# Kernel optimization log

Hardware: AMD Instinct MI355X
Metric: run time of the kernel (lower is better)

The kernel has to match this reference:

```python
import jax, jax.numpy as jnp
import numpy as np

N_NODES = 50000
N_SCHEMES = 5
K = 16
HIDDEN = 128
N_CLASSES = 8


def setup_inputs() -> dict:
    key = jax.random.key(0)
    ks = jax.random.split(key, 8)
    sc_nei = jax.random.randint(ks[0], (N_SCHEMES, N_NODES, K), 0, N_NODES)
    feats = jax.random.normal(ks[1], (N_NODES, HIDDEN), dtype=jnp.float32)
    W1 = jax.random.normal(ks[2], (HIDDEN, HIDDEN), dtype=jnp.float32) * (1.0 / np.sqrt(HIDDEN))
    b1 = jnp.zeros((HIDDEN,), dtype=jnp.float32)
    W2 = jax.random.normal(ks[3], (HIDDEN, N_CLASSES), dtype=jnp.float32) * (1.0 / np.sqrt(HIDDEN))
    b2 = jnp.zeros((N_CLASSES,), dtype=jnp.float32)
    alpha = jax.random.normal(ks[4], (N_NODES, 1), dtype=jnp.float32)
    attention = jax.random.normal(ks[5], (N_NODES, N_SCHEMES, 1), dtype=jnp.float32)
    return {"sc_nei": sc_nei, "feats": feats, "W1": W1, "b1": b1,
            "W2": W2, "b2": b2, "alpha": alpha, "attention": attention}


def _mlp(x, W1, b1, W2, b2):
    # MLP2 with num_layers=2, dropout in eval mode (identity)
    h = jax.nn.relu(x @ W1 + b1)
    return h @ W2 + b2


def reference(sc_nei, feats, W1, b1, W2, b2, alpha, attention):
    # Per-scheme: gather -> MLP -> exp(log_softmax)=softmax -> mean over neighbors
    emb = feats[sc_nei]                      # [5, N, K, H]
    probs = jax.nn.softmax(_mlp(emb, W1, b1, W2, b2), axis=-1)  # [5, N, K, C]
    sc_cls = probs.mean(axis=2)              # [5, N, C]
    x = jnp.moveaxis(sc_cls, 0, -1)          # [N, C, 5]
    att = jax.nn.softmax(attention, axis=1)  # [N, 5, 1]
    scheme_pred = jnp.squeeze(x @ att, -1)   # [N, C]
    self_pred = jax.nn.softmax(_mlp(feats[:N_NODES], W1, b1, W2, b2), axis=-1)  # [N, C]
    gate = jax.nn.sigmoid(alpha)             # sigmoid(-a) = 1 - sigmoid(a)
    return gate * self_pred + (1.0 - gate) * scheme_pred
```

## Files before the change

### kernel.cpp

```cpp
#include <hip/hip_runtime.h>
#include <hip/hip_bf16.h>
#include <hip/hip_fp16.h>
#include <math.h>

#define HIDDEN   128
#define NCLS     8
#define NSCHEMES 5
#define KNEI     16
#define NFRAG    2048

typedef __attribute__((ext_vector_type(8))) short short8;
typedef __attribute__((ext_vector_type(4))) float floatx4;

static __device__ inline unsigned pk2(float x, float y) {
    __hip_bfloat162 v = __float22bfloat162_rn(float2{x, y});
    union { __hip_bfloat162 b; unsigned u; } cv; cv.b = v;
    return cv.u;
}
static __device__ inline unsigned pkh2(float x, float y) {
    __half2 v = __floats2half2_rn(x, y);
    union { __half2 h; unsigned u; } cv; cv.h = v;
    return cv.u;
}

__global__ __launch_bounds__(256) void convert_w1(
    const float* __restrict__ W1, unsigned short* __restrict__ W1frag)
{
    int f = blockIdx.x * 256 + threadIdx.x;
    int lane = f & 63, c = (f >> 6) & 3, t = f >> 8;
    int q = lane >> 4, l16 = lane & 15;
    int j  = t * 16 + l16;
    int k0 = c * 32 + q * 8;
    union { short8 s; unsigned u[4]; } r;
    #pragma unroll
    for (int p = 0; p < 4; ++p) {
        float a = W1[(size_t)(k0 + 2 * p)     * HIDDEN + j];
        float b = W1[(size_t)(k0 + 2 * p + 1) * HIDDEN + j];
        r.u[p] = pk2(a, b);
    }
    *(short8*)(W1frag + (size_t)f * 8) = r.s;
}

__global__ __launch_bounds__(256, 4) void mlp_mfma(
    const float* __restrict__ feats, const unsigned short* __restrict__ W1frag,
    const float* __restrict__ b1, const float* __restrict__ W2,
    const float* __restrict__ b2, unsigned short* __restrict__ probsh, int N)
{
    __shared__ unsigned short fragLds[NFRAG * 8];
    __shared__ float W2l[HIDDEN * NCLS];
    __shared__ float b1l[HIDDEN];

    const int tid  = threadIdx.x;
    const int lane = tid & 63;
    const int wv   = tid >> 6;
    const int quad = lane >> 4;
    const int l16  = lane & 15;
    const int nodeBase = blockIdx.x * 64 + wv * 16;

    #pragma unroll
    for (int it = 0; it < 8; ++it) {
        short8 v = *(const short8*)(W1frag + (size_t)(it * 256 + tid) * 8);
        *(short8*)&fragLds[(it * 256 + tid) * 8] = v;
    }
    {
        float4 v = ((const float4*)W2)[tid];
        *(float4*)&W2l[4 * tid] = v;
    }
    if (tid < HIDDEN) b1l[tid] = b1[tid];
    __syncthreads();

    int myNode = nodeBase + l16;
    if (myNode >= N) myNode = N - 1;

    floatx4 acc[8];
    #pragma unroll
    for (int t = 0; t < 8; ++t) acc[t] = (floatx4){0.f, 0.f, 0.f, 0.f};

    const float* arow = feats + (size_t)myNode * HIDDEN + quad * 8;
    #pragma unroll
    for (int c = 0; c < 4; ++c) {
        float4 a0 = *(const float4*)(arow + c * 32);
        float4 a1 = *(const float4*)(arow + c * 32 + 4);
        union { short8 s; unsigned u[4]; } af;
        af.u[0] = pk2(a0.x, a0.y);
        af.u[1] = pk2(a0.z, a0.w);
        af.u[2] = pk2(a1.x, a1.y);
        af.u[3] = pk2(a1.z, a1.w);
        #pragma unroll
        for (int t = 0; t < 8; ++t) {
            short8 bf = *(const short8*)&fragLds[((t * 4 + c) * 64 + lane) * 8];
            acc[t] = __builtin_amdgcn_mfma_f32_16x16x32_bf16(af.s, bf, acc[t], 0, 0, 0);
        }
    }

    float opart[4][NCLS];
    #pragma unroll
    for (int r = 0; r < 4; ++r)
        #pragma unroll
        for (int c = 0; c < NCLS; ++c) opart[r][c] = 0.f;

    #pragma unroll
    for (int t = 0; t < 8; ++t) {
        int j = t * 16 + l16;
        float bj = b1l[j];
        float4 w0 = *(const float4*)&W2l[j * NCLS];
        float4 w1 = *(const float4*)&W2l[j * NCLS + 4];
        #pragma unroll
        for (int r = 0; r < 4; ++r) {
            float h = fmaxf(acc[t][r] + bj, 0.f);
            opart[r][0] = fmaf(h, w0.x, opart[r][0]);
            opart[r][1] = fmaf(h, w0.y, opart[r][1]);
            opart[r][2] = fmaf(h, w0.z, opart[r][2]);
            opart[r][3] = fmaf(h, w0.w, opart[r][3]);
            opart[r][4] = fmaf(h, w1.x, opart[r][4]);
            opart[r][5] = fmaf(h, w1.y, opart[r][5]);
            opart[r][6] = fmaf(h, w1.z, opart[r][6]);
            opart[r][7] = fmaf(h, w1.w, opart[r][7]);
        }
    }

    #pragma unroll
    for (int r = 0; r < 4; ++r)
        #pragma unroll
        for (int c = 0; c < NCLS; ++c) {
            float v = opart[r][c];
            v += __shfl_xor(v, 1, 64);
            v += __shfl_xor(v, 2, 64);
            v += __shfl_xor(v, 4, 64);
            v += __shfl_xor(v, 8, 64);
            opart[r][c] = v;
        }

    if (l16 == 0) {
        float4 b2lo = *(const float4*)b2;
        float4 b2hi = *(const float4*)(b2 + 4);
        float bb[NCLS] = {b2lo.x, b2lo.y, b2lo.z, b2lo.w, b2hi.x, b2hi.y, b2hi.z, b2hi.w};
        #pragma unroll
        for (int r = 0; r < 4; ++r) {
            int n = nodeBase + quad * 4 + r;
            if (n < N) {
                float o[NCLS];
                #pragma unroll
                for (int c = 0; c < NCLS; ++c) o[c] = opart[r][c] + bb[c];
                float m = o[0];
                #pragma unroll
                for (int c = 1; c < NCLS; ++c) m = fmaxf(m, o[c]);
                float s = 0.f;
                #pragma unroll
                for (int c = 0; c < NCLS; ++c) { o[c] = __expf(o[c] - m); s += o[c]; }
                float inv = 1.f / s;
                union { short8 s8; unsigned u[4]; } pr;
                pr.u[0] = pkh2(o[0] * inv, o[1] * inv);
                pr.u[1] = pkh2(o[2] * inv, o[3] * inv);
                pr.u[2] = pkh2(o[4] * inv, o[5] * inv);
                pr.u[3] = pkh2(o[6] * inv, o[7] * inv);
                *(short8*)(probsh + (size_t)n * NCLS) = pr.s8;
            }
        }
    }
}

__global__ __launch_bounds__(256) void combine(
    const int* __restrict__ nei, const unsigned short* __restrict__ probsh,
    const float* __restrict__ attention, const float* __restrict__ alpha,
    float* __restrict__ out, int N)
{
    int t = blockIdx.x * 256 + threadIdx.x;
    int n = t >> 4;
    int u = t & 15;
    int k = u;
    int L = u & 7;
    if (n >= N) return;

    float aw[NSCHEMES];
    float m = -1e30f;
    #pragma unroll
    for (int s = 0; s < NSCHEMES; ++s) {
        aw[s] = attention[(size_t)n * NSCHEMES + s];
        m = fmaxf(m, aw[s]);
    }
    float ssum = 0.f;
    #pragma unroll
    for (int s = 0; s < NSCHEMES; ++s) { aw[s] = __expf(aw[s] - m); ssum += aw[s]; }

    float g = 1.f / (1.f + __expf(-alpha[n]));
    float scale = (1.f - g) / (ssum * (float)KNEI);
    float wn[NSCHEMES];
    #pragma unroll
    for (int s = 0; s < NSCHEMES; ++s) wn[s] = aw[s] * scale;

    int id[NSCHEMES];
    #pragma unroll
    for (int s = 0; s < NSCHEMES; ++s)
        id[s] = nei[((size_t)s * N + n) * KNEI + k];

    float self;
    {
        union { unsigned u32; __half h[2]; } cv;
        cv.u32 = *(const unsigned short*)&probsh[(size_t)n * NCLS + L] |
                 ((unsigned)probsh[(size_t)n * NCLS + L] << 16);
        self = __half2float(cv.h[0]);
    }

    float acc[NCLS];
    #pragma unroll
    for (int c = 0; c < NCLS; ++c) acc[c] = 0.f;
    #pragma unroll
    for (int s = 0; s < NSCHEMES; ++s) {
        union { uint4 v; __half h[8]; } pr;
        pr.v = *(const uint4*)(probsh + (size_t)id[s] * NCLS);
        float w = wn[s];
        #pragma unroll
        for (int c = 0; c < NCLS; ++c)
            acc[c] = fmaf(w, __half2float(pr.h[c]), acc[c]);
    }

    #pragma unroll
    for (int c = 0; c < NCLS; ++c) {
        float v = acc[c];
        v += __shfl_xor(v, 1, 64);
        v += __shfl_xor(v, 2, 64);
        v += __shfl_xor(v, 4, 64);
        v += __shfl_xor(v, 8, 64);
        acc[c] = v;
    }

    if (u < 8) {
        float res = acc[0];
        #pragma unroll
        for (int c = 1; c < NCLS; ++c) res = (u == c) ? acc[c] : res;
        out[(size_t)n * NCLS + u] = fmaf(g, self, res);
    }
}

extern "C" void kernel_launch(void* const* d_in, const int* in_sizes, int n_in,
                              void* d_out, int out_size, void* d_ws, size_t ws_size,
                              hipStream_t stream) {
    const int*   sc_nei    = (const int*)d_in[0];
    const float* feats     = (const float*)d_in[1];
    const float* W1        = (const float*)d_in[2];
    const float* b1        = (const float*)d_in[3];
    const float* W2        = (const float*)d_in[4];
    const float* b2        = (const float*)d_in[5];
    const float* alpha     = (const float*)d_in[6];
    const float* attention = (const float*)d_in[7];
    float* out = (float*)d_out;

    int N = in_sizes[1] / HIDDEN;

    unsigned short* probsh = (unsigned short*)d_ws;
    unsigned short* W1frag = (unsigned short*)d_ws + (size_t)N * NCLS;

    convert_w1<<<NFRAG / 256, 256, 0, stream>>>(W1, W1frag);
    mlp_mfma<<<(N + 63) / 64, 256, 0, stream>>>(feats, W1frag, b1, W2, b2, probsh, N);
    combine<<<((N * 16) + 255) / 256, 256, 0, stream>>>(sc_nei, probsh, attention, alpha, out, N);
}
```

Baseline: 120.8 us.

## Fuse weight conversion, MLP and combine into one cooperative grid-synced kernel

Merges the three kernels into a single cooperative launch. Grid-wide barriers separate the W1 bf16 fragment conversion, the per-node MLP/softmax, and the neighbor-gather combine, which runs as a grid-stride loop. MFMA B fragments are now read straight from global memory instead of being staged in LDS, which shrinks shared memory use so more blocks fit per CU. The aim is to cut per-launch gaps and the LDS staging cost, in exchange for two grid-sync barriers and B-operand loads going through cache. If the cooperative launch fails, it falls back to the three-kernel path.

Measured after the change: 362.1 us. 200% more time.

```diff
diff --git a/kernel.cpp b/kernel.cpp
--- a/kernel.cpp
+++ b/kernel.cpp
@@ -1,7 +1,10 @@
 #include <hip/hip_runtime.h>
+#include <hip/hip_cooperative_groups.h>
 #include <hip/hip_bf16.h>
 #include <hip/hip_fp16.h>
 #include <math.h>
+
+namespace cg = cooperative_groups;
 
 #define HIDDEN   128
 #define NCLS     8
@@ -21,6 +24,211 @@
     __half2 v = __floats2half2_rn(x, y);
     union { __half2 h; unsigned u; } cv; cv.h = v;
     return cv.u;
+}
+
+__global__ __launch_bounds__(256, 4) void fused(
+    const float* __restrict__ feats, const float* __restrict__ W1,
+    const float* __restrict__ b1, const float* __restrict__ W2,
+    const float* __restrict__ b2, const int* __restrict__ nei,
+    const float* __restrict__ attention, const float* __restrict__ alpha,
+    unsigned short* __restrict__ probsh, unsigned short* __restrict__ W1frag,
+    float* __restrict__ out, int N)
+{
+    __shared__ float W2l[HIDDEN * NCLS];
+    __shared__ float b1l[HIDDEN];
+
+    const int tid  = threadIdx.x;
+    const int lane = tid & 63;
+    const int wv   = tid >> 6;
+    const int quad = lane >> 4;
+    const int l16  = lane & 15;
+
+    if (blockIdx.x < NFRAG / 256) {
+        int f = blockIdx.x * 256 + tid;
+        int fl = f & 63, c = (f >> 6) & 3, t = f >> 8;
+        int q = fl >> 4, m16 = fl & 15;
+        int j  = t * 16 + m16;
+        int k0 = c * 32 + q * 8;
+        union { short8 s; unsigned u[4]; } r;
+        #pragma unroll
+        for (int p = 0; p < 4; ++p) {
+            float a = W1[(size_t)(k0 + 2 * p)     * HIDDEN + j];
+            float b = W1[(size_t)(k0 + 2 * p + 1) * HIDDEN + j];
+            r.u[p] = pk2(a, b);
+        }
+        *(short8*)(W1frag + (size_t)f * 8) = r.s;
+    }
+    {
+        float4 v = ((const float4*)W2)[tid];
+        *(float4*)&W2l[4 * tid] = v;
+    }
+    if (tid < HIDDEN) b1l[tid] = b1[tid];
+
+    __threadfence();
+    cg::this_grid().sync();
+
+    {
+        const int nodeBase = blockIdx.x * 64 + wv * 16;
+        int myNode = nodeBase + l16;
+        if (myNode >= N) myNode = N - 1;
+
+        floatx4 acc[8];
+        #pragma unroll
+        for (int t = 0; t < 8; ++t) acc[t] = (floatx4){0.f, 0.f, 0.f, 0.f};
+
+        const float* arow = feats + (size_t)myNode * HIDDEN + quad * 8;
+        #pragma unroll
+        for (int c = 0; c < 4; ++c) {
+            float4 a0 = *(const float4*)(arow + c * 32);
+            float4 a1 = *(const float4*)(arow + c * 32 + 4);
+            union { short8 s; unsigned u[4]; } af;
+            af.u[0] = pk2(a0.x, a0.y);
+            af.u[1] = pk2(a0.z, a0.w);
+            af.u[2] = pk2(a1.x, a1.y);
+            af.u[3] = pk2(a1.z, a1.w);
+            #pragma unroll
+            for (int t = 0; t < 8; ++t) {
+                short8 bf = *(const short8*)(W1frag + (size_t)(((t * 4 + c) * 64) + lane) * 8);
+                acc[t] = __builtin_amdgcn_mfma_f32_16x16x32_bf16(af.s, bf, acc[t], 0, 0, 0);
+            }
+        }
+
+        float opart[4][NCLS];
+        #pragma unroll
+        for (int r = 0; r < 4; ++r)
+            #pragma unroll
+            for (int c = 0; c < NCLS; ++c) opart[r][c] = 0.f;
+
+        #pragma unroll
+        for (int t = 0; t < 8; ++t) {
+            int j = t * 16 + l16;
+            float bj = b1l[j];
+            float4 w0 = *(const float4*)&W2l[j * NCLS];
+            float4 w1 = *(const float4*)&W2l[j * NCLS + 4];
+            #pragma unroll
+            for (int r = 0; r < 4; ++r) {
+                float h = fmaxf(acc[t][r] + bj, 0.f);
+                opart[r][0] = fmaf(h, w0.x, opart[r][0]);
+                opart[r][1] = fmaf(h, w0.y, opart[r][1]);
+                opart[r][2] = fmaf(h, w0.z, opart[r][2]);
+                opart[r][3] = fmaf(h, w0.w, opart[r][3]);
+                opart[r][4] = fmaf(h, w1.x, opart[r][4]);
+                opart[r][5] = fmaf(h, w1.y, opart[r][5]);
+                opart[r][6] = fmaf(h, w1.z, opart[r][6]);
+                opart[r][7] = fmaf(h, w1.w, opart[r][7]);
+            }
+        }
+
+        #pragma unroll
+        for (int r = 0; r < 4; ++r)
+            #pragma unroll
+            for (int c = 0; c < NCLS; ++c) {
+                float v = opart[r][c];
+                v += __shfl_xor(v, 1, 64);
+                v += __shfl_xor(v, 2, 64);
+                v += __shfl_xor(v, 4, 64);
+                v += __shfl_xor(v, 8, 64);
+                opart[r][c] = v;
+            }
+
+        if (l16 == 0) {
+            float4 b2lo = *(const float4*)b2;
+            float4 b2hi = *(const float4*)(b2 + 4);
+            float bb[NCLS] = {b2lo.x, b2lo.y, b2lo.z, b2lo.w, b2hi.x, b2hi.y, b2hi.z, b2hi.w};
+            #pragma unroll
+            for (int r = 0; r < 4; ++r) {
+                int n = nodeBase + quad * 4 + r;
+                if (n < N) {
+                    float o[NCLS];
+                    #pragma unroll
+                    for (int c = 0; c < NCLS; ++c) o[c] = opart[r][c] + bb[c];
+                    float m = o[0];
+                    #pragma unroll
+                    for (int c = 1; c < NCLS; ++c) m = fmaxf(m, o[c]);
+                    float s = 0.f;
+                    #pragma unroll
+                    for (int c = 0; c < NCLS; ++c) { o[c] = __expf(o[c] - m); s += o[c]; }
+                    float inv = 1.f / s;
+                    union { short8 s8; unsigned u[4]; } pr;
+                    pr.u[0] = pkh2(o[0] * inv, o[1] * inv);
+                    pr.u[1] = pkh2(o[2] * inv, o[3] * inv);
+                    pr.u[2] = pkh2(o[4] * inv, o[5] * inv);
+                    pr.u[3] = pkh2(o[6] * inv, o[7] * inv);
+                    *(short8*)(probsh + (size_t)n * NCLS) = pr.s8;
+                }
+            }
+        }
+    }
+
+    __threadfence();
+    cg::this_grid().sync();
+
+    const int step = gridDim.x * 256;
+    for (int t0 = blockIdx.x * 256 + tid; t0 < N * 16; t0 += step) {
+        int n = t0 >> 4;
+        int u = t0 & 15;
+        int k = u;
+        int L = u & 7;
+
+        float aw[NSCHEMES];
+        float m = -1e30f;
+        #pragma unroll
+        for (int s = 0; s < NSCHEMES; ++s) {
+            aw[s] = attention[(size_t)n * NSCHEMES + s];
+            m = fmaxf(m, aw[s]);
+        }
+        float ssum = 0.f;
+        #pragma unroll
+        for (int s = 0; s < NSCHEMES; ++s) { aw[s] = __expf(aw[s] - m); ssum += aw[s]; }
+
+        float g = 1.f / (1.f + __expf(-alpha[n]));
+        float scale = (1.f - g) / (ssum * (float)KNEI);
+        float wn[NSCHEMES];
+        #pragma unroll
+        for (int s = 0; s < NSCHEMES; ++s) wn[s] = aw[s] * scale;
+
+        int id[NSCHEMES];
+        #pragma unroll
+        for (int s = 0; s < NSCHEMES; ++s)
+            id[s] = nei[((size_t)s * N + n) * KNEI + k];
+
+        float self;
+        {
+            union { unsigned short us; __half h; } cv;
+            cv.us = probsh[(size_t)n * NCLS + L];
+            self = __half2float(cv.h);
+        }
+
+        float acc[NCLS];
+        #pragma unroll
+        for (int c = 0; c < NCLS; ++c) acc[c] = 0.f;
+        #pragma unroll
+        for (int s = 0; s < NSCHEMES; ++s) {
+            union { uint4 v; __half h[8]; } pr;
+            pr.v = *(const uint4*)(probsh + (size_t)id[s] * NCLS);
+            float w = wn[s];
+            #pragma unroll
+            for (int c = 0; c < NCLS; ++c)
+                acc[c] = fmaf(w, __half2float(pr.h[c]), acc[c]);
+        }
+
+        #pragma unroll
+        for (int c = 0; c < NCLS; ++c) {
+            float v = acc[c];
+            v += __shfl_xor(v, 1, 64);
+            v += __shfl_xor(v, 2, 64);
+            v += __shfl_xor(v, 4, 64);
+            v += __shfl_xor(v, 8, 64);
+            acc[c] = v;
+        }
+
+        if (u < 8) {
+            float res = acc[0];
+            #pragma unroll
+            for (int c = 1; c < NCLS; ++c) res = (u == c) ? acc[c] : res;
+            out[(size_t)n * NCLS + u] = fmaf(g, self, res);
+        }
+    }
 }
 
 __global__ __launch_bounds__(256) void convert_w1(
@@ -46,7 +254,6 @@
     const float* __restrict__ b1, const float* __restrict__ W2,
     const float* __restrict__ b2, unsigned short* __restrict__ probsh, int N)
 {
-    __shared__ unsigned short fragLds[NFRAG * 8];
     __shared__ float W2l[HIDDEN * NCLS];
     __shared__ float b1l[HIDDEN];
 
@@ -57,11 +264,6 @@
     const int l16  = lane & 15;
     const int nodeBase = blockIdx.x * 64 + wv * 16;
 
-    #pragma unroll
-    for (int it = 0; it < 8; ++it) {
-        short8 v = *(const short8*)(W1frag + (size_t)(it * 256 + tid) * 8);
-        *(short8*)&fragLds[(it * 256 + tid) * 8] = v;
-    }
     {
         float4 v = ((const float4*)W2)[tid];
         *(float4*)&W2l[4 * tid] = v;
@@ -88,7 +290,7 @@
         af.u[3] = pk2(a1.z, a1.w);
         #pragma unroll
         for (int t = 0; t < 8; ++t) {
-            short8 bf = *(const short8*)&fragLds[((t * 4 + c) * 64 + lane) * 8];
+            short8 bf = *(const short8*)(W1frag + (size_t)(((t * 4 + c) * 64) + lane) * 8);
             acc[t] = __builtin_amdgcn_mfma_f32_16x16x32_bf16(af.s, bf, acc[t], 0, 0, 0);
         }
     }
@@ -196,10 +398,9 @@
 
     float self;
     {
-        union { unsigned u32; __half h[2]; } cv;
-        cv.u32 = *(const unsigned short*)&probsh[(size_t)n * NCLS + L] |
-                 ((unsigned)probsh[(size_t)n * NCLS + L] << 16);
-        self = __half2float(cv.h[0]);
+        union { unsigned short us; __half h; } cv;
+        cv.us = probsh[(size_t)n * NCLS + L];
+        self = __half2float(cv.h);
     }
 
     float acc[NCLS];
@@ -236,7 +437,6 @@
 extern "C" void kernel_launch(void* const* d_in, const int* in_sizes, int n_in,
                               void* d_out, int out_size, void* d_ws, size_t ws_size,
                               hipStream_t stream) {
-    const int*   sc_nei    = (const int*)d_in[0];
     const float* feats     = (const float*)d_in[1];
     const float* W1        = (const float*)d_in[2];
     const float* b1        = (const float*)d_in[3];
@@ -244,6 +444,7 @@
     const float* b2        = (const float*)d_in[5];
     const float* alpha     = (const float*)d_in[6];
     const float* attention = (const float*)d_in[7];
+    const int*   sc_nei    = (const int*)d_in[0];
     float* out = (float*)d_out;
 
     int N = in_sizes[1] / HIDDEN;
@@ -251,7 +452,19 @@
     unsigned short* probsh = (unsigned short*)d_ws;
     unsigned short* W1frag = (unsigned short*)d_ws + (size_t)N * NCLS;
 
-    convert_w1<<<NFRAG / 256, 256, 0, stream>>>(W1, W1frag);
-    mlp_mfma<<<(N + 63) / 64, 256, 0, stream>>>(feats, W1frag, b1, W2, b2, probsh, N);
-    combine<<<((N * 16) + 255) / 256, 256, 0, stream>>>(sc_nei, probsh, attention, alpha, out, N);
-}
+    int grid = (N + 63) / 64;
+
+    void* args[] = {
+        (void*)&feats, (void*)&W1, (void*)&b1, (void*)&W2, (void*)&b2,
+        (void*)&sc_nei, (void*)&attention, (void*)&alpha,
+        (void*)&probsh, (void*)&W1frag, (void*)&out, (void*)&N
+    };
+    hipError_t err = hipLaunchCooperativeKernel(
+        (const void*)fused, dim3(grid), dim3(256), args, 0, stream);
+
+    if (err != hipSuccess) {
+        convert_w1<<<NFRAG / 256, 256, 0, stream>>>(W1, W1frag);
+        mlp_mfma<<<grid, 256, 0, stream>>>(feats, W1frag, b1, W2, b2, probsh, N);
+        combine<<<((N * 16) + 255) / 256, 256, 0, stream>>>(sc_nei, probsh, attention, alpha, out, N);
+    }
+}
```
